# Kernel tuning notes

Measured on AMD Instinct MI355X. Metric: run time of the kernel, lower is better.

## Reference

```python
import jax, jax.numpy as jnp
import numpy as np

N = 4096        # number of sparse voxel tokens (single sequence)
C = 1024        # channels
H = 16          # num_heads
D = C // H      # head_dim = 64
FREQ_DIM = D // 2 // 3   # 10 rotary freqs per spatial axis
PAD = D // 2 - 3 * FREQ_DIM  # 2 identity-padded complex pairs


def setup_inputs() -> dict:
    key = jax.random.key(0)
    ks = jax.random.split(key, 6)
    s_in = 1.0 / np.sqrt(C)
    x = jax.random.normal(ks[0], (N, C), jnp.float32)
    coords = jax.random.randint(ks[1], (N, 3), 0, 64, dtype=jnp.int32)
    W_qkv = jax.random.normal(ks[2], (C, 3 * C), jnp.float32) * s_in
    b_qkv = jnp.zeros((3 * C,), jnp.float32)
    gamma_q = jnp.ones((H, D), jnp.float32)
    gamma_k = jnp.ones((H, D), jnp.float32)
    W_out = jax.random.normal(ks[3], (C, C), jnp.float32) * s_in
    b_out = jnp.zeros((C,), jnp.float32)
    return {"x": x, "coords": coords, "W_qkv": W_qkv, "b_qkv": b_qkv,
            "gamma_q": gamma_q, "gamma_k": gamma_k, "W_out": W_out, "b_out": b_out}


def _rms_norm(t, gamma):
    # F.normalize(x, dim=-1) * gamma * sqrt(D), computed in fp32
    t = t.astype(jnp.float32)
    nrm = jnp.maximum(jnp.linalg.norm(t, axis=-1, keepdims=True), 1e-12)
    return (t / nrm) * gamma * np.float32(np.sqrt(D))


def _rope_phases(coords):
    # freqs: rope_freq[0] / rope_freq[1]**(i/freq_dim)
    freqs = 1.0 / (10000.0 ** (jnp.arange(FREQ_DIM, dtype=jnp.float32) / FREQ_DIM))
    ph = coords.astype(jnp.float32).reshape(-1)[:, None] * freqs   # [N*3, FREQ_DIM]
    ph = ph.reshape(N, 3 * FREQ_DIM)
    # pad with zero-phase (identity rotation) to head_dim//2
    cos = jnp.concatenate([jnp.cos(ph), jnp.ones((N, PAD), jnp.float32)], axis=-1)
    sin = jnp.concatenate([jnp.sin(ph), jnp.zeros((N, PAD), jnp.float32)], axis=-1)
    return cos, sin


def _rope_apply(t, cos, sin):
    # complex rotation on consecutive pairs of the head dim
    tr = t.reshape(N, H, D // 2, 2)
    t0, t1 = tr[..., 0], tr[..., 1]
    c, s = cos[:, None, :], sin[:, None, :]
    o0 = t0 * c - t1 * s
    o1 = t0 * s + t1 * c
    return jnp.stack([o0, o1], axis=-1).reshape(N, H, D)


def reference(x, coords, W_qkv, b_qkv, gamma_q, gamma_k, W_out, b_out):
    qkv = (x @ W_qkv + b_qkv).reshape(N, 3, H, D)
    q, k, v = qkv[:, 0], qkv[:, 1], qkv[:, 2]
    q = _rms_norm(q, gamma_q)
    k = _rms_norm(k, gamma_k)
    cos, sin = _rope_phases(coords)
    q = _rope_apply(q, cos, sin)
    k = _rope_apply(k, cos, sin)
    scores = jnp.einsum('nhd,mhd->hnm', q, k) / np.float32(np.sqrt(D))
    attn = jax.nn.softmax(scores, axis=-1)
    h = jnp.einsum('hnm,mhd->nhd', attn, v).reshape(N, C)
    return h @ W_out + b_out
```

## Files before the change

### kernel.cpp

```cpp
#include <hip/hip_runtime.h>

#define DEVI __device__ __forceinline__

typedef __attribute__((ext_vector_type(8))) short bf16x8;
typedef __attribute__((ext_vector_type(4))) float f32x4;
typedef __attribute__((ext_vector_type(16))) float f32x16;

DEVI ushort f2bf(float f) {
  union { float f; unsigned u; } v; v.f = f;
  unsigned u = v.u;
  unsigned r = (u + 0x7FFFu + ((u >> 16) & 1u)) >> 16;
  return (ushort)r;
}
DEVI float bf2f(ushort h) {
  union { unsigned u; float f; } v; v.u = ((unsigned)h) << 16;
  return v.f;
}
DEVI unsigned pkbf(float lo, float hi) {
  unsigned r;
  asm("v_cvt_pk_bf16_f32 %0, %1, %2" : "=v"(r) : "v"(lo), "v"(hi));
  return r;
}
DEVI float exp2v(float x) {
#if __has_builtin(__builtin_amdgcn_exp2f)
  return __builtin_amdgcn_exp2f(x);
#else
  return exp2f(x);
#endif
}

DEVI void gload_lds16(const ushort* g, ushort* l) {
  __builtin_amdgcn_global_load_lds((const __attribute__((address_space(1))) void*)g,
                                   (__attribute__((address_space(3))) void*)l, 16, 0, 0);
}

DEVI void xcd_swz(int& bx, int& by) {
  const int nx = gridDim.x;
  const int flat = blockIdx.x + blockIdx.y * nx;
  const int cpx = (nx * gridDim.y) >> 3;
  const int swz = (flat & 7) * cpx + (flat >> 3);
  bx = swz % nx;
  by = swz / nx;
}

__global__ __launch_bounds__(256) void prep(const float* __restrict__ x,
                                            ushort* __restrict__ xb,
                                            const float* __restrict__ Wq,
                                            ushort* __restrict__ wtq,
                                            const float* __restrict__ Wo,
                                            ushort* __restrict__ wto) {
  __shared__ ushort tile[64][65];
  const int bid = blockIdx.x, t = threadIdx.x;
  if (bid < 4096) {
    int i = bid * 256 + t;
    const float4 v = ((const float4*)x)[i];
    uint2 o;
    o.x = (unsigned)f2bf(v.x) | ((unsigned)f2bf(v.y) << 16);
    o.y = (unsigned)f2bf(v.z) | ((unsigned)f2bf(v.w) << 16);
    ((uint2*)xb)[i] = o;
    return;
  }
  const float* in;
  ushort* out;
  int R, Cc, bx, by;
  if (bid < 4864) {
    in = Wq; out = wtq; R = 1024; Cc = 3072;
    bx = (bid - 4096) % 48; by = (bid - 4096) / 48;
  } else {
    in = Wo; out = wto; R = 1024; Cc = 1024;
    bx = (bid - 4864) % 16; by = (bid - 4864) / 16;
  }
  const int r0 = by * 64, c0 = bx * 64;
  for (int i = 0; i < 16; ++i) {
    int rr = i * 4 + (t >> 6), cc = t & 63;
    tile[rr][cc] = f2bf(in[(size_t)(r0 + rr) * Cc + c0 + cc]);
  }
  __syncthreads();
  for (int i = 0; i < 16; ++i) {
    int cc = i * 4 + (t >> 6), rr = t & 63;
    out[(size_t)(c0 + cc) * R + r0 + rr] = tile[rr][cc];
  }
}

__global__ __launch_bounds__(256, 2) void gemm_qkv(const ushort* __restrict__ A,
                                                   const ushort* __restrict__ Bt,
                                                   const float* __restrict__ bias,
                                                   ushort* __restrict__ O) {
  __shared__ ushort lds[2 * 20480];
  const int tid = threadIdx.x;
  const int w = tid >> 6, l = tid & 63;
  const int flat = blockIdx.x;
  const int xcd = flat & 7, slot = flat >> 3;
  const int bm = (xcd >> 1) * 8 + (slot >> 3);
  const int bn = (xcd & 1) * 8 + (slot & 7);
  const int m0 = bm * 128, n0 = bn * 192;
  const int wn = w * 48;
  const int lc = l & 15, lg = l >> 4;

  const int lrow = l >> 3;
  const int lcol = ((l & 7) ^ lrow) * 8;
  const ushort* pA[4];
  const ushort* pB[6];
#pragma unroll
  for (int i = 0; i < 4; ++i)
    pA[i] = A + (size_t)(m0 + (w * 4 + i) * 8 + lrow) * 1024 + lcol;
#pragma unroll
  for (int i = 0; i < 6; ++i)
    pB[i] = Bt + (size_t)(n0 + (w * 6 + i) * 8 + lrow) * 1024 + lcol;

  ushort* cur = lds;
  ushort* nxt = lds + 20480;

#pragma unroll
  for (int i = 0; i < 4; ++i) gload_lds16(pA[i], cur + (w * 4 + i) * 512);
#pragma unroll
  for (int i = 0; i < 6; ++i) gload_lds16(pB[i], cur + 8192 + (w * 6 + i) * 512);
  asm volatile("s_waitcnt vmcnt(0)" ::: "memory");
  __builtin_amdgcn_s_barrier();
  __builtin_amdgcn_sched_barrier(0);

  f32x4 acc[8][3];
#pragma unroll
  for (int i = 0; i < 8; ++i)
#pragma unroll
    for (int j = 0; j < 3; ++j) acc[i][j] = (f32x4){0.f, 0.f, 0.f, 0.f};

  const int aoff = lc * 64;
  const int boff = 8192 + (wn + lc) * 64;
  const int roph0 = ((0 + lg) ^ (lc & 7)) * 8;
  const int roph1 = ((4 + lg) ^ (lc & 7)) * 8;

  for (int t = 0; t < 16; ++t) {
    if (t < 15) {
#pragma unroll
      for (int i = 0; i < 4; ++i) gload_lds16(pA[i] + (t + 1) * 64, nxt + (w * 4 + i) * 512);
#pragma unroll
      for (int i = 0; i < 6; ++i) gload_lds16(pB[i] + (t + 1) * 64, nxt + 8192 + (w * 6 + i) * 512);
    }
    bf16x8 bfr[2][3];
#pragma unroll
    for (int fc = 0; fc < 3; ++fc) {
      bfr[0][fc] = *(const bf16x8*)(cur + boff + fc * 1024 + roph0);
      bfr[1][fc] = *(const bf16x8*)(cur + boff + fc * 1024 + roph1);
    }
    __builtin_amdgcn_s_setprio(1);
#pragma unroll
    for (int kc = 0; kc < 2; ++kc) {
      const int roph = kc ? roph1 : roph0;
      bf16x8 af[8];
#pragma unroll
      for (int fr = 0; fr < 8; ++fr)
        af[fr] = *(const bf16x8*)(cur + aoff + fr * 1024 + roph);
#pragma unroll
      for (int fr = 0; fr < 8; ++fr)
#pragma unroll
        for (int fc = 0; fc < 3; ++fc)
          acc[fr][fc] = __builtin_amdgcn_mfma_f32_16x16x32_bf16(af[fr], bfr[kc][fc], acc[fr][fc], 0, 0, 0);
    }
    __builtin_amdgcn_s_setprio(0);
    if (t < 15) {
      asm volatile("s_waitcnt vmcnt(0) lgkmcnt(0)" ::: "memory");
      __builtin_amdgcn_s_barrier();
      __builtin_amdgcn_sched_barrier(0);
      ushort* tp = cur; cur = nxt; nxt = tp;
    }
  }

  const int lr = lg * 4;
#pragma unroll
  for (int fc = 0; fc < 3; ++fc) {
    const int col = n0 + wn + fc * 16 + lc;
    const float bv = bias[col];
    const int grp = col >> 10, hh = (col >> 6) & 15, dd = col & 63;
    if (grp < 2) {
      size_t base = (size_t)grp * (16 * 4096 * 64) + (size_t)hh * (4096 * 64) + dd;
#pragma unroll
      for (int fr = 0; fr < 8; ++fr)
#pragma unroll
        for (int r = 0; r < 4; ++r) {
          int row = m0 + fr * 16 + lr + r;
          O[base + (size_t)row * 64] = f2bf(acc[fr][fc][r] + bv);
        }
    } else {
      size_t base = (size_t)2 * (16 * 4096 * 64) + ((size_t)hh * 64 + dd) * 4096;
#pragma unroll
      for (int fr = 0; fr < 8; ++fr)
#pragma unroll
        for (int r = 0; r < 4; ++r) {
          int row = m0 + fr * 16 + lr + r;
          O[base + row] = f2bf(acc[fr][fc][r] + bv);
        }
    }
  }
}

__global__ __launch_bounds__(256) void gemm_out(const ushort* __restrict__ A,
                                                const ushort* __restrict__ Bt,
                                                const float* __restrict__ bias,
                                                float* __restrict__ O,
                                                int M, int Nn, int K) {
  __shared__ ushort As[2][128 * 32];
  __shared__ ushort Bs[2][128 * 32];
  const int tid = threadIdx.x;
  const int w = tid >> 6, l = tid & 63;
  int bx, by;
  xcd_swz(bx, by);
  const int m0 = by * 128, n0 = bx * 128;
  const int wm = (w >> 1) * 64, wn = (w & 1) * 64;
  const int lc = l & 15, lg = l >> 4;

  f32x4 acc[4][4];
  for (int i = 0; i < 4; ++i)
    for (int j = 0; j < 4; ++j) acc[i][j] = (f32x4){0.f, 0.f, 0.f, 0.f};

  const int srow = w * 32 + (l >> 2);
  const int scol = (l & 3) * 8;
  const ushort* gA = A + (size_t)(m0 + srow) * K + scol;
  const ushort* gB = Bt + (size_t)(n0 + srow) * K + scol;

  for (int k0 = 0; k0 < K; k0 += 64) {
#pragma unroll
    for (int s = 0; s < 2; ++s) {
      gload_lds16(gA + k0 + 32 * s,                  &As[s][(w * 32 + 0) * 32]);
      gload_lds16(gA + k0 + 32 * s + (size_t)16 * K, &As[s][(w * 32 + 16) * 32]);
      gload_lds16(gB + k0 + 32 * s,                  &Bs[s][(w * 32 + 0) * 32]);
      gload_lds16(gB + k0 + 32 * s + (size_t)16 * K, &Bs[s][(w * 32 + 16) * 32]);
    }
    __syncthreads();
#pragma unroll
    for (int s = 0; s < 2; ++s) {
      bf16x8 af[4], bfr[4];
      for (int mi = 0; mi < 4; ++mi)
        af[mi] = *(const bf16x8*)(&As[s][(wm + mi * 16 + lc) * 32 + lg * 8]);
      for (int ni = 0; ni < 4; ++ni)
        bfr[ni] = *(const bf16x8*)(&Bs[s][(wn + ni * 16 + lc) * 32 + lg * 8]);
      for (int mi = 0; mi < 4; ++mi)
        for (int ni = 0; ni < 4; ++ni)
          acc[mi][ni] = __builtin_amdgcn_mfma_f32_16x16x32_bf16(af[mi], bfr[ni], acc[mi][ni], 0, 0, 0);
    }
    __syncthreads();
  }

  const int lr = lg * 4;
  for (int ni = 0; ni < 4; ++ni) {
    int col = n0 + wn + ni * 16 + lc;
    float bv = bias[col];
    for (int mi = 0; mi < 4; ++mi)
      for (int r = 0; r < 4; ++r)
        O[(size_t)(m0 + wm + mi * 16 + lr + r) * Nn + col] = acc[mi][ni][r] + bv;
  }
}

DEVI void nr_one(ushort* B, const float* g, size_t base, int h, int l16,
                 float c0a, float s0a, float c1a, float s1a, float extra) {
  unsigned u0 = *(const unsigned*)(B + base + 2 * l16);
  unsigned u1 = *(const unsigned*)(B + base + 32 + 2 * l16);
  float t00 = bf2f((ushort)u0), t01 = bf2f((ushort)(u0 >> 16));
  float t10 = bf2f((ushort)u1), t11 = bf2f((ushort)(u1 >> 16));
  float ss = t00 * t00 + t01 * t01 + t10 * t10 + t11 * t11;
  for (int d = 1; d < 16; d <<= 1) ss += __shfl_xor(ss, d, 16);
  float scl = 8.f / fmaxf(sqrtf(ss), 1e-12f);
  scl *= extra;
  float g00 = g[h * 64 + 2 * l16], g01 = g[h * 64 + 2 * l16 + 1];
  float g10 = g[h * 64 + 32 + 2 * l16], g11 = g[h * 64 + 33 + 2 * l16];
  float q00 = t00 * scl * g00, q01 = t01 * scl * g01;
  float q10 = t10 * scl * g10, q11 = t11 * scl * g11;
  float o00 = q00 * c0a - q01 * s0a, o01 = q00 * s0a + q01 * c0a;
  float o10 = q10 * c1a - q11 * s1a, o11 = q10 * s1a + q11 * c1a;
  *(unsigned*)(B + base + 2 * l16) = (unsigned)f2bf(o00) | ((unsigned)f2bf(o01) << 16);
  *(unsigned*)(B + base + 32 + 2 * l16) = (unsigned)f2bf(o10) | ((unsigned)f2bf(o11) << 16);
}

__global__ __launch_bounds__(256) void norm_rope(ushort* __restrict__ Qb,
                                                 ushort* __restrict__ Kb,
                                                 const int* __restrict__ coords,
                                                 const float* __restrict__ gq,
                                                 const float* __restrict__ gk) {
  const int n = blockIdx.x, t = threadIdx.x;
  const int h = t >> 4, l16 = t & 15;
  const float L2_10K_D10 = 1.3287712379549449f;
  float c0a, s0a, c1a, s1a;
  {
    int p = l16;
    int j = p / 10, fi = p - j * 10;
    float freq = exp2f(-(float)fi * L2_10K_D10);
    float ang = (float)coords[n * 3 + j] * freq;
    c0a = cosf(ang); s0a = sinf(ang);
  }
  {
    int p = l16 + 16;
    if (p < 30) {
      int j = p / 10, fi = p - j * 10;
      float freq = exp2f(-(float)fi * L2_10K_D10);
      float ang = (float)coords[n * 3 + j] * freq;
      c1a = cosf(ang); s1a = sinf(ang);
    } else { c1a = 1.f; s1a = 0.f; }
  }
  const size_t base = ((size_t)h * 4096 + n) * 64;
  nr_one(Qb, gq, base, h, l16, c0a, s0a, c1a, s1a, 0.125f * 1.4426950408889634f);
  nr_one(Kb, gk, base, h, l16, c0a, s0a, c1a, s1a, 1.0f);
}

DEVI void attn_step(const bf16x8 (&ck)[8], const bf16x8 (&cv)[8], const bf16x8 (&qf)[4],
                    f32x16& o0, f32x16& o1, f32x4& rs) {
  f32x16 s0, s1;
#pragma unroll
  for (int r = 0; r < 16; ++r) { s0[r] = 0.f; s1[r] = 0.f; }
#pragma unroll
  for (int c = 0; c < 4; ++c) {
    s0 = __builtin_amdgcn_mfma_f32_32x32x16_bf16(ck[c],     qf[c], s0, 0, 0, 0);
    s1 = __builtin_amdgcn_mfma_f32_32x32x16_bf16(ck[c + 4], qf[c], s1, 0, 0, 0);
  }
#pragma unroll
  for (int r = 0; r < 16; ++r) { s0[r] = exp2v(s0[r]); }
#pragma unroll
  for (int r = 0; r < 16; ++r) { s1[r] = exp2v(s1[r]); }
#pragma unroll
  for (int r = 0; r < 16; r += 4) {
    rs[0] += s0[r] + s1[r];
    rs[1] += s0[r + 1] + s1[r + 1];
    rs[2] += s0[r + 2] + s1[r + 2];
    rs[3] += s0[r + 3] + s1[r + 3];
  }
  union { unsigned u[4]; bf16x8 v; } pb[4];
  {
    auto r0 = __builtin_amdgcn_permlane32_swap(pkbf(s0[0], s0[1]), pkbf(s0[4], s0[5]), false, false);
    auto r1 = __builtin_amdgcn_permlane32_swap(pkbf(s0[2], s0[3]), pkbf(s0[6], s0[7]), false, false);
    pb[0].u[0] = r0[0]; pb[0].u[1] = r1[0]; pb[0].u[2] = r0[1]; pb[0].u[3] = r1[1];
    auto r2 = __builtin_amdgcn_permlane32_swap(pkbf(s0[8], s0[9]), pkbf(s0[12], s0[13]), false, false);
    auto r3 = __builtin_amdgcn_permlane32_swap(pkbf(s0[10], s0[11]), pkbf(s0[14], s0[15]), false, false);
    pb[1].u[0] = r2[0]; pb[1].u[1] = r3[0]; pb[1].u[2] = r2[1]; pb[1].u[3] = r3[1];
    auto r4 = __builtin_amdgcn_permlane32_swap(pkbf(s1[0], s1[1]), pkbf(s1[4], s1[5]), false, false);
    auto r5 = __builtin_amdgcn_permlane32_swap(pkbf(s1[2], s1[3]), pkbf(s1[6], s1[7]), false, false);
    pb[2].u[0] = r4[0]; pb[2].u[1] = r5[0]; pb[2].u[2] = r4[1]; pb[2].u[3] = r5[1];
    auto r6 = __builtin_amdgcn_permlane32_swap(pkbf(s1[8], s1[9]), pkbf(s1[12], s1[13]), false, false);
    auto r7 = __builtin_amdgcn_permlane32_swap(pkbf(s1[10], s1[11]), pkbf(s1[14], s1[15]), false, false);
    pb[3].u[0] = r6[0]; pb[3].u[1] = r7[0]; pb[3].u[2] = r6[1]; pb[3].u[3] = r7[1];
  }
#pragma unroll
  for (int c = 0; c < 4; ++c) {
    o0 = __builtin_amdgcn_mfma_f32_32x32x16_bf16(cv[c],     pb[c].v, o0, 0, 0, 0);
    o1 = __builtin_amdgcn_mfma_f32_32x32x16_bf16(cv[c + 4], pb[c].v, o1, 0, 0, 0);
  }
}

__global__ __launch_bounds__(256, 2) void attn_fwd(const ushort* __restrict__ Qb,
                                                   const ushort* __restrict__ Kb,
                                                   const ushort* __restrict__ Vt,
                                                   ushort* __restrict__ attnb) {
  __shared__ ushort Ks[2][4096];
  __shared__ ushort Vs[2][4096];

  const int flat = blockIdx.x + (blockIdx.y << 5);
  const int swz = (flat & 7) * 64 + (flat >> 3);
  const int bx = swz & 31, h = swz >> 5;

  const int l = threadIdx.x & 63, w = threadIdx.x >> 6;
  const int q = l & 31, hi = l >> 5;
  const int q0 = bx * 128 + w * 32;

  const ushort* qrow = Qb + ((size_t)h * 4096 + q0 + q) * 64 + hi * 8;
  bf16x8 qf[4];
#pragma unroll
  for (int c = 0; c < 4; ++c) qf[c] = *(const bf16x8*)(qrow + 16 * c);

  f32x16 o0, o1;
#pragma unroll
  for (int r = 0; r < 16; ++r) { o0[r] = 0.f; o1[r] = 0.f; }
  f32x4 rs = (f32x4){0.f, 0.f, 0.f, 0.f};

  const ushort* gK = Kb + ((size_t)h * 4096 + l) * 64 + 2 * w * 8;
  const ushort* gV = Vt + ((size_t)h * 64 + l) * 4096 + 2 * w * 8;

  ushort* Kc = &Ks[0][0]; ushort* Vc = &Vs[0][0];
  ushort* Kn = &Ks[1][0]; ushort* Vn = &Vs[1][0];

  gload_lds16(gK, Kc + 2 * w * 512);
  gload_lds16(gK + 8, Kc + (2 * w + 1) * 512);
  gload_lds16(gV, Vc + 2 * w * 512);
  gload_lds16(gV + 8, Vc + (2 * w + 1) * 512);
  asm volatile("s_waitcnt vmcnt(0)" ::: "memory");
  __builtin_amdgcn_s_barrier();
  __builtin_amdgcn_sched_barrier(0);

  const int lbase = hi * 512 + q * 8;
  for (int t = 0; t < 63; ++t) {
    const ushort* sK = gK + (size_t)(t + 1) * 64 * 64;
    const ushort* sV = gV + (t + 1) * 64;
    gload_lds16(sK, Kn + 2 * w * 512);
    gload_lds16(sK + 8, Kn + (2 * w + 1) * 512);
    gload_lds16(sV, Vn + 2 * w * 512);
    gload_lds16(sV + 8, Vn + (2 * w + 1) * 512);

    bf16x8 k[8], v[8];
#pragma unroll
    for (int c = 0; c < 4; ++c) {
      k[c]     = *(const bf16x8*)(Kc + lbase + c * 1024);
      k[c + 4] = *(const bf16x8*)(Kc + lbase + c * 1024 + 256);
      v[c]     = *(const bf16x8*)(Vc + lbase + c * 1024);
      v[c + 4] = *(const bf16x8*)(Vc + lbase + c * 1024 + 256);
    }
    __builtin_amdgcn_s_setprio(1);
    attn_step(k, v, qf, o0, o1, rs);
    __builtin_amdgcn_s_setprio(0);

    asm volatile("s_waitcnt vmcnt(0) lgkmcnt(0)" ::: "memory");
    __builtin_amdgcn_s_barrier();
    __builtin_amdgcn_sched_barrier(0);
    ushort* tp;
    tp = Kc; Kc = Kn; Kn = tp;
    tp = Vc; Vc = Vn; Vn = tp;
  }
  {
    bf16x8 k[8], v[8];
#pragma unroll
    for (int c = 0; c < 4; ++c) {
      k[c]     = *(const bf16x8*)(Kc + lbase + c * 1024);
      k[c + 4] = *(const bf16x8*)(Kc + lbase + c * 1024 + 256);
      v[c]     = *(const bf16x8*)(Vc + lbase + c * 1024);
      v[c + 4] = *(const bf16x8*)(Vc + lbase + c * 1024 + 256);
    }
    attn_step(k, v, qf, o0, o1, rs);
  }

  float lsum = (rs[0] + rs[1]) + (rs[2] + rs[3]);
  lsum += __shfl_xor(lsum, 32);
  const float inv = 1.f / lsum;
  ushort* orow = attnb + (size_t)(q0 + q) * 1024 + h * 64;
#pragma unroll
  for (int dt = 0; dt < 2; ++dt) {
    const f32x16& oo = dt ? o1 : o0;
#pragma unroll
    for (int g = 0; g < 4; ++g)
#pragma unroll
      for (int p2 = 0; p2 < 2; ++p2) {
        int r = g * 4 + p2 * 2;
        unsigned pk = pkbf(oo[r] * inv, oo[r + 1] * inv);
        *(unsigned*)(orow + dt * 32 + g * 8 + 4 * hi + p2 * 2) = pk;
      }
  }
}

extern "C" void kernel_launch(void* const* d_in, const int* in_sizes, int n_in,
                              void* d_out, int out_size, void* d_ws, size_t ws_size,
                              hipStream_t stream) {
  const float* x      = (const float*)d_in[0];
  const int*   coords = (const int*)d_in[1];
  const float* W_qkv  = (const float*)d_in[2];
  const float* b_qkv  = (const float*)d_in[3];
  const float* gq     = (const float*)d_in[4];
  const float* gk     = (const float*)d_in[5];
  const float* W_out  = (const float*)d_in[6];
  const float* b_out  = (const float*)d_in[7];
  float* out = (float*)d_out;

  char* ws = (char*)d_ws;
  ushort* xb    = (ushort*)(ws);
  ushort* wtqkv = (ushort*)(ws + (8u << 20));
  ushort* wtout = (ushort*)(ws + (14u << 20));
  ushort* Qb    = (ushort*)(ws + (16u << 20));
  ushort* Kb    = (ushort*)(ws + (24u << 20));
  ushort* Vt    = (ushort*)(ws + (32u << 20));
  ushort* attnb = (ushort*)(ws + (40u << 20));

  prep<<<5120, 256, 0, stream>>>(x, xb, W_qkv, wtqkv, W_out, wtout);
  gemm_qkv<<<512, 256, 0, stream>>>(xb, wtqkv, b_qkv, Qb);
  norm_rope<<<4096, 256, 0, stream>>>(Qb, Kb, coords, gq, gk);
  attn_fwd<<<dim3(32, 16), 256, 0, stream>>>(Qb, Kb, Vt, attnb);
  gemm_out<<<dim3(8, 32), 256, 0, stream>>>(attnb, wtout, b_out, out, 4096, 1024, 1024);
}
```

Baseline: 153.2 us.

## Split attention over KV halves with a separate combine kernel

Adds a split-KV attention kernel that launches twice as many blocks, each covering half of the key/value sequence. Each block writes unnormalized fp32 partial outputs and row sums to workspace. A combine kernel then adds the two halves, normalizes and converts to bf16. This aims to raise occupancy and spread work over more CUs on the 256-CU device, at the cost of 32 MB of extra fp32 traffic and one more launch. It appears to rely on softmax without a running max (fixed offset), so partials can be summed directly.

```diff
diff --git a/kernel.cpp b/kernel.cpp
--- a/kernel.cpp
+++ b/kernel.cpp
@@ -344,6 +344,124 @@
   }
 }
 
+__global__ __launch_bounds__(256, 4) void attn_split(const ushort* __restrict__ Qb,
+                                                     const ushort* __restrict__ Kb,
+                                                     const ushort* __restrict__ Vt,
+                                                     float* __restrict__ Opart,
+                                                     float* __restrict__ Lpart) {
+  __shared__ ushort Ks[2][4096];
+  __shared__ ushort Vs[2][4096];
+
+  const int flat = blockIdx.x + (blockIdx.y << 5) + (blockIdx.z << 9);
+  const int swz = (flat & 7) * 128 + (flat >> 3);
+  const int bx = swz & 31, h = (swz >> 5) & 15, half = swz >> 9;
+  const int kv0 = half * 2048;
+
+  const int l = threadIdx.x & 63, w = threadIdx.x >> 6;
+  const int q = l & 31, hi = l >> 5;
+  const int q0 = bx * 128 + w * 32;
+
+  const ushort* qrow = Qb + ((size_t)h * 4096 + q0 + q) * 64 + hi * 8;
+  bf16x8 qf[4];
+#pragma unroll
+  for (int c = 0; c < 4; ++c) qf[c] = *(const bf16x8*)(qrow + 16 * c);
+
+  f32x16 o0, o1;
+#pragma unroll
+  for (int r = 0; r < 16; ++r) { o0[r] = 0.f; o1[r] = 0.f; }
+  f32x4 rs = (f32x4){0.f, 0.f, 0.f, 0.f};
+
+  const ushort* gK = Kb + ((size_t)h * 4096 + kv0 + l) * 64 + 2 * w * 8;
+  const ushort* gV = Vt + ((size_t)h * 64 + l) * 4096 + kv0 + 2 * w * 8;
+
+  ushort* Kc = &Ks[0][0]; ushort* Vc = &Vs[0][0];
+  ushort* Kn = &Ks[1][0]; ushort* Vn = &Vs[1][0];
+
+  gload_lds16(gK, Kc + 2 * w * 512);
+  gload_lds16(gK + 8, Kc + (2 * w + 1) * 512);
+  gload_lds16(gV, Vc + 2 * w * 512);
+  gload_lds16(gV + 8, Vc + (2 * w + 1) * 512);
+  asm volatile("s_waitcnt vmcnt(0)" ::: "memory");
+  __builtin_amdgcn_s_barrier();
+  __builtin_amdgcn_sched_barrier(0);
+
+  const int lbase = hi * 512 + q * 8;
+  for (int t = 0; t < 31; ++t) {
+    const ushort* sK = gK + (size_t)(t + 1) * 64 * 64;
+    const ushort* sV = gV + (t + 1) * 64;
+    gload_lds16(sK, Kn + 2 * w * 512);
+    gload_lds16(sK + 8, Kn + (2 * w + 1) * 512);
+    gload_lds16(sV, Vn + 2 * w * 512);
+    gload_lds16(sV + 8, Vn + (2 * w + 1) * 512);
+
+    bf16x8 k[8], v[8];
+#pragma unroll
+    for (int c = 0; c < 4; ++c) {
+      k[c]     = *(const bf16x8*)(Kc + lbase + c * 1024);
+      k[c + 4] = *(const bf16x8*)(Kc + lbase + c * 1024 + 256);
+      v[c]     = *(const bf16x8*)(Vc + lbase + c * 1024);
+      v[c + 4] = *(const bf16x8*)(Vc + lbase + c * 1024 + 256);
+    }
+    __builtin_amdgcn_s_setprio(1);
+    attn_step(k, v, qf, o0, o1, rs);
+    __builtin_amdgcn_s_setprio(0);
+
+    asm volatile("s_waitcnt vmcnt(0) lgkmcnt(0)" ::: "memory");
+    __builtin_amdgcn_s_barrier();
+    __builtin_amdgcn_sched_barrier(0);
+    ushort* tp;
+    tp = Kc; Kc = Kn; Kn = tp;
+    tp = Vc; Vc = Vn; Vn = tp;
+  }
+  {
+    bf16x8 k[8], v[8];
+#pragma unroll
+    for (int c = 0; c < 4; ++c) {
+      k[c]     = *(const bf16x8*)(Kc + lbase + c * 1024);
+      k[c + 4] = *(const bf16x8*)(Kc + lbase + c * 1024 + 256);
+      v[c]     = *(const bf16x8*)(Vc + lbase + c * 1024);
+      v[c + 4] = *(const bf16x8*)(Vc + lbase + c * 1024 + 256);
+    }
+    attn_step(k, v, qf, o0, o1, rs);
+  }
+
+  float lsum = (rs[0] + rs[1]) + (rs[2] + rs[3]);
+  lsum += __shfl_xor(lsum, 32);
+  if (hi == 0) Lpart[(size_t)half * 65536 + h * 4096 + q0 + q] = lsum;
+
+  float* orow = Opart + (size_t)half * (4096 * 1024) + (size_t)(q0 + q) * 1024 + h * 64;
+#pragma unroll
+  for (int dt = 0; dt < 2; ++dt) {
+    const f32x16& oo = dt ? o1 : o0;
+#pragma unroll
+    for (int g = 0; g < 4; ++g)
+#pragma unroll
+      for (int p2 = 0; p2 < 2; ++p2) {
+        int r = g * 4 + p2 * 2;
+        float2 val = make_float2(oo[r], oo[r + 1]);
+        *(float2*)(orow + dt * 32 + g * 8 + 4 * hi + p2 * 2) = val;
+      }
+  }
+}
+
+__global__ __launch_bounds__(256) void attn_combine(const float* __restrict__ Opart,
+                                                    const float* __restrict__ Lpart,
+                                                    ushort* __restrict__ attnb) {
+  const int idx = (blockIdx.x * 256 + threadIdx.x) * 8;
+  const int n = idx >> 10, c0 = idx & 1023, h = c0 >> 6;
+  const float inv = 1.f / (Lpart[h * 4096 + n] + Lpart[65536 + h * 4096 + n]);
+  const float4* p1 = (const float4*)(Opart + idx);
+  const float4* p2 = (const float4*)(Opart + (size_t)(4096 * 1024) + idx);
+  float4 a0 = p1[0], a1 = p1[1], b0 = p2[0], b1 = p2[1];
+  uint2 w0, w1;
+  w0.x = pkbf((a0.x + b0.x) * inv, (a0.y + b0.y) * inv);
+  w0.y = pkbf((a0.z + b0.z) * inv, (a0.w + b0.w) * inv);
+  w1.x = pkbf((a1.x + b1.x) * inv, (a1.y + b1.y) * inv);
+  w1.y = pkbf((a1.z + b1.z) * inv, (a1.w + b1.w) * inv);
+  ((uint2*)(attnb + idx))[0] = w0;
+  ((uint2*)(attnb + idx))[1] = w1;
+}
+
 __global__ __launch_bounds__(256, 2) void attn_fwd(const ushort* __restrict__ Qb,
                                                    const ushort* __restrict__ Kb,
                                                    const ushort* __restrict__ Vt,
@@ -462,10 +580,17 @@
   ushort* Kb    = (ushort*)(ws + (24u << 20));
   ushort* Vt    = (ushort*)(ws + (32u << 20));
   ushort* attnb = (ushort*)(ws + (40u << 20));
+  float*  Opart = (float*)(ws + (48u << 20));
+  float*  Lpart = (float*)(ws + (80u << 20));
 
   prep<<<5120, 256, 0, stream>>>(x, xb, W_qkv, wtqkv, W_out, wtout);
   gemm_qkv<<<512, 256, 0, stream>>>(xb, wtqkv, b_qkv, Qb);
   norm_rope<<<4096, 256, 0, stream>>>(Qb, Kb, coords, gq, gk);
-  attn_fwd<<<dim3(32, 16), 256, 0, stream>>>(Qb, Kb, Vt, attnb);
+  if (ws_size >= ((size_t)81 << 20)) {
+    attn_split<<<dim3(32, 16, 2), 256, 0, stream>>>(Qb, Kb, Vt, Opart, Lpart);
+    attn_combine<<<16384, 256, 0, stream>>>(Opart, Lpart, attnb);
+  } else {
+    attn_fwd<<<dim3(32, 16), 256, 0, stream>>>(Qb, Kb, Vt, attnb);
+  }
   gemm_out<<<dim3(8, 32), 256, 0, stream>>>(attnb, wtout, b_out, out, 4096, 1024, 1024);
 }
```

Result: slower. 309.1 us (+101.7%).

## Split attention KV range across wave pairs and combine partial outputs in LDS

Applied to the files above, without the earlier changes.

The attention kernel now processes 64 queries per block instead of 128, with two waves per query tile each covering half of the KV sequence (split-K). The partial outputs and row sums are reduced through shared memory at the end. The grid doubles to 1024 blocks and the launch bounds rise to 4 blocks per CU, which is meant to improve occupancy and CU utilisation on a grid that was previously only 512 blocks. In exchange, each KV tile is now 32 keys, so per-step MFMA work shrinks relative to barrier and load overhead, and a final LDS reduction is added.

```diff
diff --git a/kernel.cpp b/kernel.cpp
--- a/kernel.cpp
+++ b/kernel.cpp
@@ -301,63 +301,23 @@
   nr_one(Kb, gk, base, h, l16, c0a, s0a, c1a, s1a, 1.0f);
 }
 
-DEVI void attn_step(const bf16x8 (&ck)[8], const bf16x8 (&cv)[8], const bf16x8 (&qf)[4],
-                    f32x16& o0, f32x16& o1, f32x4& rs) {
-  f32x16 s0, s1;
-#pragma unroll
-  for (int r = 0; r < 16; ++r) { s0[r] = 0.f; s1[r] = 0.f; }
-#pragma unroll
-  for (int c = 0; c < 4; ++c) {
-    s0 = __builtin_amdgcn_mfma_f32_32x32x16_bf16(ck[c],     qf[c], s0, 0, 0, 0);
-    s1 = __builtin_amdgcn_mfma_f32_32x32x16_bf16(ck[c + 4], qf[c], s1, 0, 0, 0);
-  }
-#pragma unroll
-  for (int r = 0; r < 16; ++r) { s0[r] = exp2v(s0[r]); }
-#pragma unroll
-  for (int r = 0; r < 16; ++r) { s1[r] = exp2v(s1[r]); }
-#pragma unroll
-  for (int r = 0; r < 16; r += 4) {
-    rs[0] += s0[r] + s1[r];
-    rs[1] += s0[r + 1] + s1[r + 1];
-    rs[2] += s0[r + 2] + s1[r + 2];
-    rs[3] += s0[r + 3] + s1[r + 3];
-  }
-  union { unsigned u[4]; bf16x8 v; } pb[4];
-  {
-    auto r0 = __builtin_amdgcn_permlane32_swap(pkbf(s0[0], s0[1]), pkbf(s0[4], s0[5]), false, false);
-    auto r1 = __builtin_amdgcn_permlane32_swap(pkbf(s0[2], s0[3]), pkbf(s0[6], s0[7]), false, false);
-    pb[0].u[0] = r0[0]; pb[0].u[1] = r1[0]; pb[0].u[2] = r0[1]; pb[0].u[3] = r1[1];
-    auto r2 = __builtin_amdgcn_permlane32_swap(pkbf(s0[8], s0[9]), pkbf(s0[12], s0[13]), false, false);
-    auto r3 = __builtin_amdgcn_permlane32_swap(pkbf(s0[10], s0[11]), pkbf(s0[14], s0[15]), false, false);
-    pb[1].u[0] = r2[0]; pb[1].u[1] = r3[0]; pb[1].u[2] = r2[1]; pb[1].u[3] = r3[1];
-    auto r4 = __builtin_amdgcn_permlane32_swap(pkbf(s1[0], s1[1]), pkbf(s1[4], s1[5]), false, false);
-    auto r5 = __builtin_amdgcn_permlane32_swap(pkbf(s1[2], s1[3]), pkbf(s1[6], s1[7]), false, false);
-    pb[2].u[0] = r4[0]; pb[2].u[1] = r5[0]; pb[2].u[2] = r4[1]; pb[2].u[3] = r5[1];
-    auto r6 = __builtin_amdgcn_permlane32_swap(pkbf(s1[8], s1[9]), pkbf(s1[12], s1[13]), false, false);
-    auto r7 = __builtin_amdgcn_permlane32_swap(pkbf(s1[10], s1[11]), pkbf(s1[14], s1[15]), false, false);
-    pb[3].u[0] = r6[0]; pb[3].u[1] = r7[0]; pb[3].u[2] = r6[1]; pb[3].u[3] = r7[1];
-  }
-#pragma unroll
-  for (int c = 0; c < 4; ++c) {
-    o0 = __builtin_amdgcn_mfma_f32_32x32x16_bf16(cv[c],     pb[c].v, o0, 0, 0, 0);
-    o1 = __builtin_amdgcn_mfma_f32_32x32x16_bf16(cv[c + 4], pb[c].v, o1, 0, 0, 0);
-  }
-}
-
-__global__ __launch_bounds__(256, 2) void attn_fwd(const ushort* __restrict__ Qb,
+__global__ __launch_bounds__(256, 4) void attn_fwd(const ushort* __restrict__ Qb,
                                                    const ushort* __restrict__ Kb,
                                                    const ushort* __restrict__ Vt,
                                                    ushort* __restrict__ attnb) {
-  __shared__ ushort Ks[2][4096];
-  __shared__ ushort Vs[2][4096];
-
-  const int flat = blockIdx.x + (blockIdx.y << 5);
-  const int swz = (flat & 7) * 64 + (flat >> 3);
-  const int bx = swz & 31, h = swz >> 5;
+  __shared__ ushort Ks[2][2][2048];
+  __shared__ ushort Vs[2][2][2048];
+
+  const int flat = blockIdx.x + (blockIdx.y << 6);
+  const int swz = (flat & 7) * 128 + (flat >> 3);
+  const int bx = swz & 63, h = swz >> 6;
 
   const int l = threadIdx.x & 63, w = threadIdx.x >> 6;
   const int q = l & 31, hi = l >> 5;
-  const int q0 = bx * 128 + w * 32;
+  const int qt = w & 1, half = w >> 1;
+  const int q0 = bx * 64 + qt * 32;
+  const int kv0 = half * 2048;
+  const int lp = qt * 64 + l;
 
   const ushort* qrow = Qb + ((size_t)h * 4096 + q0 + q) * 64 + hi * 8;
   bf16x8 qf[4];
@@ -369,75 +329,119 @@
   for (int r = 0; r < 16; ++r) { o0[r] = 0.f; o1[r] = 0.f; }
   f32x4 rs = (f32x4){0.f, 0.f, 0.f, 0.f};
 
-  const ushort* gK = Kb + ((size_t)h * 4096 + l) * 64 + 2 * w * 8;
-  const ushort* gV = Vt + ((size_t)h * 64 + l) * 4096 + 2 * w * 8;
-
-  ushort* Kc = &Ks[0][0]; ushort* Vc = &Vs[0][0];
-  ushort* Kn = &Ks[1][0]; ushort* Vn = &Vs[1][0];
-
-  gload_lds16(gK, Kc + 2 * w * 512);
-  gload_lds16(gK + 8, Kc + (2 * w + 1) * 512);
-  gload_lds16(gV, Vc + 2 * w * 512);
-  gload_lds16(gV + 8, Vc + (2 * w + 1) * 512);
+  const ushort* gK = Kb + ((size_t)h * 4096 + kv0 + (lp & 31)) * 64 + (lp >> 5) * 8;
+  const ushort* gV = Vt + ((size_t)h * 64 + (lp & 63)) * 4096 + kv0 + (lp >> 6) * 8;
+
+  ushort* Kc = &Ks[0][half][0]; ushort* Vc = &Vs[0][half][0];
+  ushort* Kn = &Ks[1][half][0]; ushort* Vn = &Vs[1][half][0];
+
+  gload_lds16(gK,      Kc + lp * 8);
+  gload_lds16(gK + 32, Kc + 1024 + lp * 8);
+  gload_lds16(gV,      Vc + lp * 8);
+  gload_lds16(gV + 16, Vc + 1024 + lp * 8);
   asm volatile("s_waitcnt vmcnt(0)" ::: "memory");
   __builtin_amdgcn_s_barrier();
   __builtin_amdgcn_sched_barrier(0);
 
-  const int lbase = hi * 512 + q * 8;
-  for (int t = 0; t < 63; ++t) {
-    const ushort* sK = gK + (size_t)(t + 1) * 64 * 64;
-    const ushort* sV = gV + (t + 1) * 64;
-    gload_lds16(sK, Kn + 2 * w * 512);
-    gload_lds16(sK + 8, Kn + (2 * w + 1) * 512);
-    gload_lds16(sV, Vn + 2 * w * 512);
-    gload_lds16(sV + 8, Vn + (2 * w + 1) * 512);
-
-    bf16x8 k[8], v[8];
-#pragma unroll
-    for (int c = 0; c < 4; ++c) {
-      k[c]     = *(const bf16x8*)(Kc + lbase + c * 1024);
-      k[c + 4] = *(const bf16x8*)(Kc + lbase + c * 1024 + 256);
-      v[c]     = *(const bf16x8*)(Vc + lbase + c * 1024);
-      v[c + 4] = *(const bf16x8*)(Vc + lbase + c * 1024 + 256);
-    }
+  const int kfo = hi * 256 + q * 8;
+  const int vfo = hi * 512 + q * 8;
+
+  for (int t = 0; t < 64; ++t) {
+    if (t < 63) {
+      const ushort* sK = gK + (size_t)(t + 1) * 2048;
+      const ushort* sV = gV + (t + 1) * 32;
+      gload_lds16(sK,      Kn + lp * 8);
+      gload_lds16(sK + 32, Kn + 1024 + lp * 8);
+      gload_lds16(sV,      Vn + lp * 8);
+      gload_lds16(sV + 16, Vn + 1024 + lp * 8);
+    }
+    bf16x8 k[4], va[4];
+#pragma unroll
+    for (int c = 0; c < 4; ++c) k[c] = *(const bf16x8*)(Kc + c * 512 + kfo);
+    va[0] = *(const bf16x8*)(Vc + vfo);
+    va[1] = *(const bf16x8*)(Vc + 1024 + vfo);
+    va[2] = *(const bf16x8*)(Vc + vfo + 256);
+    va[3] = *(const bf16x8*)(Vc + 1024 + vfo + 256);
+
     __builtin_amdgcn_s_setprio(1);
-    attn_step(k, v, qf, o0, o1, rs);
+    f32x16 s;
+#pragma unroll
+    for (int r = 0; r < 16; ++r) s[r] = 0.f;
+#pragma unroll
+    for (int c = 0; c < 4; ++c)
+      s = __builtin_amdgcn_mfma_f32_32x32x16_bf16(k[c], qf[c], s, 0, 0, 0);
+
+#pragma unroll
+    for (int r = 0; r < 16; ++r) s[r] = exp2v(s[r]);
+#pragma unroll
+    for (int r = 0; r < 16; r += 4) {
+      rs[0] += s[r];
+      rs[1] += s[r + 1];
+      rs[2] += s[r + 2];
+      rs[3] += s[r + 3];
+    }
+
+    union { unsigned u[4]; bf16x8 v; } pb0, pb1;
+    {
+      auto r0 = __builtin_amdgcn_permlane32_swap(pkbf(s[0], s[1]), pkbf(s[4], s[5]), false, false);
+      auto r1 = __builtin_amdgcn_permlane32_swap(pkbf(s[2], s[3]), pkbf(s[6], s[7]), false, false);
+      pb0.u[0] = r0[0]; pb0.u[1] = r1[0]; pb0.u[2] = r0[1]; pb0.u[3] = r1[1];
+      auto r2 = __builtin_amdgcn_permlane32_swap(pkbf(s[8], s[9]), pkbf(s[12], s[13]), false, false);
+      auto r3 = __builtin_amdgcn_permlane32_swap(pkbf(s[10], s[11]), pkbf(s[14], s[15]), false, false);
+      pb1.u[0] = r2[0]; pb1.u[1] = r3[0]; pb1.u[2] = r2[1]; pb1.u[3] = r3[1];
+    }
+
+    o0 = __builtin_amdgcn_mfma_f32_32x32x16_bf16(va[0], pb0.v, o0, 0, 0, 0);
+    o0 = __builtin_amdgcn_mfma_f32_32x32x16_bf16(va[1], pb1.v, o0, 0, 0, 0);
+    o1 = __builtin_amdgcn_mfma_f32_32x32x16_bf16(va[2], pb0.v, o1, 0, 0, 0);
+    o1 = __builtin_amdgcn_mfma_f32_32x32x16_bf16(va[3], pb1.v, o1, 0, 0, 0);
     __builtin_amdgcn_s_setprio(0);
 
-    asm volatile("s_waitcnt vmcnt(0) lgkmcnt(0)" ::: "memory");
-    __builtin_amdgcn_s_barrier();
-    __builtin_amdgcn_sched_barrier(0);
-    ushort* tp;
-    tp = Kc; Kc = Kn; Kn = tp;
-    tp = Vc; Vc = Vn; Vn = tp;
-  }
-  {
-    bf16x8 k[8], v[8];
-#pragma unroll
-    for (int c = 0; c < 4; ++c) {
-      k[c]     = *(const bf16x8*)(Kc + lbase + c * 1024);
-      k[c + 4] = *(const bf16x8*)(Kc + lbase + c * 1024 + 256);
-      v[c]     = *(const bf16x8*)(Vc + lbase + c * 1024);
-      v[c + 4] = *(const bf16x8*)(Vc + lbase + c * 1024 + 256);
-    }
-    attn_step(k, v, qf, o0, o1, rs);
+    if (t < 63) {
+      asm volatile("s_waitcnt vmcnt(0) lgkmcnt(0)" ::: "memory");
+      __builtin_amdgcn_s_barrier();
+      __builtin_amdgcn_sched_barrier(0);
+      ushort* tp;
+      tp = Kc; Kc = Kn; Kn = tp;
+      tp = Vc; Vc = Vn; Vn = tp;
+    }
   }
 
   float lsum = (rs[0] + rs[1]) + (rs[2] + rs[3]);
   lsum += __shfl_xor(lsum, 32);
-  const float inv = 1.f / lsum;
-  ushort* orow = attnb + (size_t)(q0 + q) * 1024 + h * 64;
-#pragma unroll
-  for (int dt = 0; dt < 2; ++dt) {
-    const f32x16& oo = dt ? o1 : o0;
-#pragma unroll
-    for (int g = 0; g < 4; ++g)
-#pragma unroll
-      for (int p2 = 0; p2 < 2; ++p2) {
-        int r = g * 4 + p2 * 2;
-        unsigned pk = pkbf(oo[r] * inv, oo[r + 1] * inv);
-        *(unsigned*)(orow + dt * 32 + g * 8 + 4 * hi + p2 * 2) = pk;
-      }
+
+  float* comb = (float*)&Ks[0][0][0];
+  float* lcmb = (float*)&Vs[0][0][0];
+  const int cl = qt * 64 + l;
+  if (half == 1) {
+#pragma unroll
+    for (int r = 0; r < 16; ++r) comb[r * 128 + cl] = o0[r];
+#pragma unroll
+    for (int r = 0; r < 16; ++r) comb[(16 + r) * 128 + cl] = o1[r];
+    lcmb[cl] = lsum;
+  }
+  __builtin_amdgcn_s_barrier();
+  if (half == 0) {
+#pragma unroll
+    for (int r = 0; r < 16; ++r) o0[r] += comb[r * 128 + cl];
+#pragma unroll
+    for (int r = 0; r < 16; ++r) o1[r] += comb[(16 + r) * 128 + cl];
+    lsum += lcmb[cl];
+
+    const float inv = 1.f / lsum;
+    ushort* orow = attnb + (size_t)(q0 + q) * 1024 + h * 64;
+#pragma unroll
+    for (int dt = 0; dt < 2; ++dt) {
+      const f32x16& oo = dt ? o1 : o0;
+#pragma unroll
+      for (int g = 0; g < 4; ++g)
+#pragma unroll
+        for (int p2 = 0; p2 < 2; ++p2) {
+          int r = g * 4 + p2 * 2;
+          unsigned pk = pkbf(oo[r] * inv, oo[r + 1] * inv);
+          *(unsigned*)(orow + dt * 32 + g * 8 + 4 * hi + p2 * 2) = pk;
+        }
+    }
   }
 }
 
@@ -466,6 +470,6 @@
   prep<<<5120, 256, 0, stream>>>(x, xb, W_qkv, wtqkv, W_out, wtout);
   gemm_qkv<<<512, 256, 0, stream>>>(xb, wtqkv, b_qkv, Qb);
   norm_rope<<<4096, 256, 0, stream>>>(Qb, Kb, coords, gq, gk);
-  attn_fwd<<<dim3(32, 16), 256, 0, stream>>>(Qb, Kb, Vt, attnb);
+  attn_fwd<<<dim3(64, 16), 256, 0, stream>>>(Qb, Kb, Vt, attnb);
   gemm_out<<<dim3(8, 32), 256, 0, stream>>>(attnb, wtout, b_out, out, 4096, 1024, 1024);
 }
```

Result: slower. 197.6 us (+29.0%).
